# Kernel optimization log

Measured on AMD Instinct MI355X. Metric: run time of the kernel, lower is better.

Reference implementation:

```python
import jax, jax.numpy as jnp
import numpy as np

DEGREE = 8


def setup_inputs() -> dict:
    key = jax.random.key(0)
    k1, k2 = jax.random.split(key)
    x = jax.random.normal(k1, (8192, 1024), dtype=jnp.float32)
    # xavier_normal-ish scale for coeffs [input_dim, output_dim, degree+1]
    std = (2.0 / (1024 + 1024)) ** 0.5
    cheby_coeffs = jax.random.normal(k2, (1024, 1024, DEGREE + 1), dtype=jnp.float32) * std
    return {"x": x, "cheby_coeffs": cheby_coeffs}


def _cheby(x, degree):
    # x: [B, I] in [-1, 1]; returns T: [B, I, degree+1]
    T = [jnp.ones_like(x), x]
    for n in range(2, degree + 1):
        T.append(2.0 * x * T[-1] - T[-2])
    return jnp.stack(T, axis=-1)


def reference(x, cheby_coeffs) -> jnp.ndarray:
    input_dim = cheby_coeffs.shape[0]
    degree = cheby_coeffs.shape[-1] - 1
    x = x.reshape(-1, input_dim)
    xmin = jnp.min(x, axis=1, keepdims=True)
    xmax = jnp.max(x, axis=1, keepdims=True)
    x = 2.0 * (x - xmin) / (xmax - xmin) - 1.0
    T = _cheby(x, degree)  # [B, I, D+1]
    y = jnp.einsum('bij,ioj->bo', T, cheby_coeffs)
    return y
```

## Files before the change

### kernel.cpp

```cpp
#include <hip/hip_runtime.h>
#include <hip/hip_bf16.h>


typedef __attribute__((ext_vector_type(8))) short bf16x8s;
typedef __attribute__((ext_vector_type(4))) float f32x4;

constexpr int BROWS = 8192;
constexpr int IDIM  = 1024;
constexpr int ODIM  = 1024;
constexpr int DEG1  = 9;
constexpr int KP    = 8;
constexpr int KD    = IDIM * KP;

__device__ __forceinline__ ushort f2bf(float f) {
  return ((__hip_bfloat16_raw)__float2bfloat16(f)).x;
}

__device__ __forceinline__ void gload_lds16(const void* g, void* l) {
  __builtin_amdgcn_global_load_lds(
      (const __attribute__((address_space(1))) unsigned int*)g,
      (__attribute__((address_space(3))) unsigned int*)l, 16, 0, 0);
}

__global__ __launch_bounds__(256) void build_a_kernel(const float* __restrict__ x,
                                                      ushort* __restrict__ A2,
                                                      float* __restrict__ bias) {
  __shared__ float red[8];
  const int b = blockIdx.x, t = threadIdx.x, lane = t & 63, wv = t >> 6;
  if (b < 4) bias[b * 256 + t] = 0.0f;
  const float* xr = x + (size_t)b * IDIM;
  const float4 v = ((const float4*)xr)[t];
  float mn = fminf(fminf(v.x, v.y), fminf(v.z, v.w));
  float mx = fmaxf(fmaxf(v.x, v.y), fmaxf(v.z, v.w));
#pragma unroll
  for (int off = 32; off >= 1; off >>= 1) {
    mn = fminf(mn, __shfl_xor(mn, off));
    mx = fmaxf(mx, __shfl_xor(mx, off));
  }
  if (lane == 0) { red[wv] = mn; red[4 + wv] = mx; }
  __syncthreads();
  mn = fminf(fminf(red[0], red[1]), fminf(red[2], red[3]));
  mx = fmaxf(fmaxf(red[4], red[5]), fmaxf(red[6], red[7]));
  const float sc = 2.0f / (mx - mn);
  const float of = -mn * sc - 1.0f;

  uint4* adst = (uint4*)(A2 + (size_t)b * KD);
#pragma unroll
  for (int c = 0; c < 4; ++c) {
    const int i = c * 256 + t;
    const float xn = fmaf(sc, xr[i], of);
    const float T2 = 2.f * xn * xn - 1.f;
    const float T3 = 2.f * xn * T2 - xn;
    const float T4 = 2.f * xn * T3 - T2;
    const float T5 = 2.f * xn * T4 - T3;
    const float T6 = 2.f * xn * T5 - T4;
    const float T7 = 2.f * xn * T6 - T5;
    const float T8 = 2.f * xn * T7 - T6;
    uint4 w;
    w.x = (uint)f2bf(xn) | ((uint)f2bf(T2) << 16);
    w.y = (uint)f2bf(T3) | ((uint)f2bf(T4) << 16);
    w.z = (uint)f2bf(T5) | ((uint)f2bf(T6) << 16);
    w.w = (uint)f2bf(T7) | ((uint)f2bf(T8) << 16);
    adst[i] = w;
  }
}

__global__ __launch_bounds__(256) void build_b_kernel(const float* __restrict__ coeffs,
                                                      ushort* __restrict__ B2T,
                                                      float* __restrict__ bias) {
  __shared__ __align__(16) ushort tile[64 * 256];
  __shared__ float lb[64];
  const int i0 = blockIdx.x * 32;
  const int o0 = blockIdx.y * 64;
  const int t  = threadIdx.x;
  if (t < 64) lb[t] = 0.0f;
  __syncthreads();
  for (int idx = t; idx < 18432; idx += 256) {
    const int i_l = idx / 576;
    const int rem = idx - i_l * 576;
    const float v = coeffs[((size_t)(i0 + i_l) * ODIM + o0) * DEG1 + rem];
    const int o_l = rem / 9;
    const int j   = rem - o_l * 9;
    if (j == 0) atomicAdd(&lb[o_l], v);
    else tile[o_l * 256 + i_l * KP + (j - 1)] = f2bf(v);
  }
  __syncthreads();
  for (int idx = t; idx < 2048; idx += 256) {
    const int o_l = idx >> 5;
    const int w   = idx & 31;
    uint4* gdst = (uint4*)(B2T + (size_t)(o0 + o_l) * KD + i0 * KP);
    gdst[w] = ((const uint4*)tile)[idx];
  }
  if (t < 64) atomicAdd(&bias[o0 + t], lb[t]);
}

__global__ __launch_bounds__(256, 2) void gemm_kernel(const ushort* __restrict__ A2,
                                                      const ushort* __restrict__ B2T,
                                                      const float* __restrict__ bias,
                                                      float* __restrict__ out) {
  constexpr int BK    = 32;
  constexpr int KT    = KD / BK;
  constexpr int ABUFU = 256 * BK;
  constexpr int BBUFU = 128 * BK;
  constexpr int BUFSZ = ABUFU + BBUFU;
  __shared__ __align__(16) ushort Sm[3 * BUFSZ];

  const int t    = threadIdx.x;
  const int lane = t & 63;
  const int wave = t >> 6;
  const int wr   = wave >> 1;
  const int wc   = wave & 1;
  const int c16  = lane & 15;
  const int quad = lane >> 4;

  const int orig = blockIdx.y * 8 + blockIdx.x;
  const int swz  = (orig & 7) * 32 + (orig >> 3);
  const int rowBase = (swz >> 3) * 256;
  const int colBase = (swz & 7) * 128;

  const int trow = t >> 2;
  const int scol = (t & 3) ^ ((t >> 3) & 3);
  const ushort* aB = A2  + (size_t)(rowBase + trow) * KD + scol * 8;
  const ushort* bB = B2T + (size_t)(colBase + trow) * KD + scol * 8;
  ushort* uA = Sm + t * 8;
  ushort* uB = Sm + ABUFU + t * 8;

  auto issA = [&](int buf, int itile, int a) {
    gload_lds16(aB + (size_t)a * (64 * KD) + (size_t)itile * BK,
                uA + buf * BUFSZ + a * 2048);
  };
  auto issB = [&](int buf, int itile, int b2) {
    gload_lds16(bB + (size_t)b2 * (64 * KD) + (size_t)itile * BK,
                uB + buf * BUFSZ + b2 * 2048);
  };

  const int cx   = (quad ^ ((c16 >> 1) & 3)) * 8;
  const int aoff = (wr * 128 + c16) * BK + cx;
  const int boff = (wc * 64 + c16) * BK + cx;

  f32x4 acc[8][4];
#pragma unroll
  for (int m = 0; m < 8; ++m)
#pragma unroll
    for (int n = 0; n < 4; ++n) acc[m][n] = (f32x4){0.f, 0.f, 0.f, 0.f};

  issA(0, 0, 0); issA(0, 0, 1); issA(0, 0, 2); issA(0, 0, 3);
  issB(0, 0, 0); issB(0, 0, 1);
  issA(1, 1, 0); issA(1, 1, 1); issA(1, 1, 2); issA(1, 1, 3);
  issB(1, 1, 0); issB(1, 1, 1);
  asm volatile("s_waitcnt vmcnt(6)" ::: "memory");
  __builtin_amdgcn_s_barrier();

  int cur = 0;
  for (int it = 0; it < KT; ++it) {
    const ushort* Asb = Sm + cur * BUFSZ;
    const ushort* Bsb = Asb + ABUFU;
    const int nb = (cur >= 1) ? cur - 1 : 2;
    const bool pf = (it < KT - 2);

    bf16x8s afr[8], bfr[4];
#pragma unroll
    for (int m = 0; m < 8; ++m)
      afr[m] = *(const bf16x8s*)&Asb[aoff + m * (16 * BK)];
#pragma unroll
    for (int n = 0; n < 4; ++n)
      bfr[n] = *(const bf16x8s*)&Bsb[boff + n * (16 * BK)];

    if (pf) {
      issA(nb, it + 2, 0); issA(nb, it + 2, 1);
      issA(nb, it + 2, 2); issA(nb, it + 2, 3);
      issB(nb, it + 2, 0); issB(nb, it + 2, 1);
    }

    __builtin_amdgcn_s_setprio(1);
#pragma unroll
    for (int m = 0; m < 8; ++m)
#pragma unroll
      for (int n = 0; n < 4; ++n)
        acc[m][n] = __builtin_amdgcn_mfma_f32_16x16x32_bf16(afr[m], bfr[n],
                                                            acc[m][n], 0, 0, 0);
    __builtin_amdgcn_s_setprio(0);

    if (pf)              { asm volatile("s_waitcnt vmcnt(6)" ::: "memory"); }
    else if (it == KT-2) { asm volatile("s_waitcnt vmcnt(0)" ::: "memory"); }
    __builtin_amdgcn_s_barrier();

    cur = (cur == 2) ? 0 : cur + 1;
  }

#pragma unroll
  for (int n = 0; n < 4; ++n) {
    const int col = colBase + wc * 64 + n * 16 + c16;
    const float bv = bias[col];
#pragma unroll
    for (int m = 0; m < 8; ++m) {
      const int r0 = rowBase + wr * 128 + m * 16 + quad * 4;
#pragma unroll
      for (int r = 0; r < 4; ++r)
        out[(size_t)(r0 + r) * ODIM + col] = acc[m][n][r] + bv;
    }
  }
}

extern "C" void kernel_launch(void* const* d_in, const int* in_sizes, int n_in,
                              void* d_out, int out_size, void* d_ws, size_t ws_size,
                              hipStream_t stream) {
  const float* x      = (const float*)d_in[0];
  const float* coeffs = (const float*)d_in[1];
  float* out = (float*)d_out;

  char* ws = (char*)d_ws;
  float*  bias = (float*)ws;
  ushort* B2T  = (ushort*)(ws + 65536);
  ushort* A2   = (ushort*)(ws + 65536 + (size_t)ODIM * KD * 2);

  build_a_kernel<<<BROWS, 256, 0, stream>>>(x, A2, bias);
  build_b_kernel<<<dim3(IDIM / 32, ODIM / 64), 256, 0, stream>>>(coeffs, B2T, bias);
  gemm_kernel<<<dim3(ODIM / 128, BROWS / 256), 256, 0, stream>>>(A2, B2T, bias, out);
}
```

Baseline: 297.5 us.

## Split K across two wave groups per block with LDS reduction

The GEMM block grows to 512 threads as two 4-wave groups. Each group runs its own triple-buffered pipeline over half of the K dimension, and the partial accumulators are combined through shared memory before the bias-added store. With one block per CU on a 256-block grid, this doubles the resident waves and gives more latency hiding for the MFMA loop. In exchange it doubles LDS use, forces one block per CU, and adds an LDS reduction step at the end.

```diff
diff --git a/kernel.cpp b/kernel.cpp
--- a/kernel.cpp
+++ b/kernel.cpp
@@ -11,6 +11,7 @@
 constexpr int DEG1  = 9;
 constexpr int KP    = 8;
 constexpr int KD    = IDIM * KP;
+constexpr int KH    = KD / 2;
 
 __device__ __forceinline__ ushort f2bf(float f) {
   return ((__hip_bfloat16_raw)__float2bfloat16(f)).x;
@@ -94,22 +95,24 @@
   if (t < 64) atomicAdd(&bias[o0 + t], lb[t]);
 }
 
-__global__ __launch_bounds__(256, 2) void gemm_kernel(const ushort* __restrict__ A2,
+__global__ __launch_bounds__(512, 1) void gemm_kernel(const ushort* __restrict__ A2,
                                                       const ushort* __restrict__ B2T,
                                                       const float* __restrict__ bias,
                                                       float* __restrict__ out) {
   constexpr int BK    = 32;
-  constexpr int KT    = KD / BK;
+  constexpr int KT    = KH / BK;
   constexpr int ABUFU = 256 * BK;
   constexpr int BBUFU = 128 * BK;
   constexpr int BUFSZ = ABUFU + BBUFU;
-  __shared__ __align__(16) ushort Sm[3 * BUFSZ];
+  __shared__ __align__(16) ushort Sm[2 * 3 * BUFSZ];
 
   const int t    = threadIdx.x;
   const int lane = t & 63;
   const int wave = t >> 6;
-  const int wr   = wave >> 1;
-  const int wc   = wave & 1;
+  const int g    = wave >> 2;
+  const int w4   = wave & 3;
+  const int wr   = w4 >> 1;
+  const int wc   = w4 & 1;
   const int c16  = lane & 15;
   const int quad = lane >> 4;
 
@@ -118,12 +121,14 @@
   const int rowBase = (swz >> 3) * 256;
   const int colBase = (swz & 7) * 128;
 
-  const int trow = t >> 2;
-  const int scol = (t & 3) ^ ((t >> 3) & 3);
-  const ushort* aB = A2  + (size_t)(rowBase + trow) * KD + scol * 8;
-  const ushort* bB = B2T + (size_t)(colBase + trow) * KD + scol * 8;
-  ushort* uA = Sm + t * 8;
-  ushort* uB = Sm + ABUFU + t * 8;
+  const int tp   = t & 255;
+  const int trow = tp >> 2;
+  const int scol = (tp & 3) ^ ((tp >> 3) & 3);
+  const ushort* aB = A2  + (size_t)(rowBase + trow) * KD + (size_t)g * KH + scol * 8;
+  const ushort* bB = B2T + (size_t)(colBase + trow) * KD + (size_t)g * KH + scol * 8;
+  ushort* SmG = Sm + g * (3 * BUFSZ);
+  ushort* uA  = SmG + tp * 8;
+  ushort* uB  = SmG + ABUFU + tp * 8;
 
   auto issA = [&](int buf, int itile, int a) {
     gload_lds16(aB + (size_t)a * (64 * KD) + (size_t)itile * BK,
@@ -153,7 +158,7 @@
 
   int cur = 0;
   for (int it = 0; it < KT; ++it) {
-    const ushort* Asb = Sm + cur * BUFSZ;
+    const ushort* Asb = SmG + cur * BUFSZ;
     const ushort* Bsb = Asb + ABUFU;
     const int nb = (cur >= 1) ? cur - 1 : 2;
     const bool pf = (it < KT - 2);
@@ -188,16 +193,33 @@
     cur = (cur == 2) ? 0 : cur + 1;
   }
 
-#pragma unroll
-  for (int n = 0; n < 4; ++n) {
-    const int col = colBase + wc * 64 + n * 16 + c16;
-    const float bv = bias[col];
-#pragma unroll
-    for (int m = 0; m < 8; ++m) {
-      const int r0 = rowBase + wr * 128 + m * 16 + quad * 4;
-#pragma unroll
-      for (int r = 0; r < 4; ++r)
-        out[(size_t)(r0 + r) * ODIM + col] = acc[m][n][r] + bv;
+  __syncthreads();
+  float* Ct = (float*)Sm;
+  if (g == 1) {
+#pragma unroll
+    for (int m = 0; m < 8; ++m)
+#pragma unroll
+      for (int n = 0; n < 4; ++n) {
+        const int lr0 = wr * 128 + m * 16 + quad * 4;
+        const int cl  = wc * 64 + n * 16 + c16;
+#pragma unroll
+        for (int r = 0; r < 4; ++r) Ct[(lr0 + r) * 128 + cl] = acc[m][n][r];
+      }
+  }
+  __syncthreads();
+  if (g == 0) {
+#pragma unroll
+    for (int n = 0; n < 4; ++n) {
+      const int cl = wc * 64 + n * 16 + c16;
+      const float bv = bias[colBase + cl];
+#pragma unroll
+      for (int m = 0; m < 8; ++m) {
+        const int lr0 = wr * 128 + m * 16 + quad * 4;
+#pragma unroll
+        for (int r = 0; r < 4; ++r)
+          out[(size_t)(rowBase + lr0 + r) * ODIM + colBase + cl] =
+              acc[m][n][r] + Ct[(lr0 + r) * 128 + cl] + bv;
+      }
     }
   }
 }
@@ -216,5 +238,5 @@
 
   build_a_kernel<<<BROWS, 256, 0, stream>>>(x, A2, bias);
   build_b_kernel<<<dim3(IDIM / 32, ODIM / 64), 256, 0, stream>>>(coeffs, B2T, bias);
-  gemm_kernel<<<dim3(ODIM / 128, BROWS / 256), 256, 0, stream>>>(A2, B2T, bias, out);
-}
+  gemm_kernel<<<dim3(ODIM / 128, BROWS / 256), 512, 0, stream>>>(A2, B2T, bias, out);
+}
```

New measurement: 293.5 us. No clear change (-1.4%).
